# Kernel tuning notes

Hardware: AMD Instinct MI355X
Metric: run time of the kernel (lower is better)

The kernel has to match this reference:

```python
import jax, jax.numpy as jnp
import numpy as np

N_OBJ, N_REG = 4096, 8192
D_HO = D_HR = 512
GATE_W = 128
E = 131072


def setup_inputs() -> dict:
    key = jax.random.key(0)
    ks = jax.random.split(key, 10)
    s = 1.0 / np.sqrt(D_HO + D_HR)
    return {
        "feature_obj": jax.random.normal(ks[0], (N_OBJ, D_HO), jnp.float32),
        "feature_region": jax.random.normal(ks[1], (N_REG, D_HR), jnp.float32),
        # edge lists (tgt, src) equivalent to np.where(select_mat > 0)
        "r2o_tgt": jnp.sort(jax.random.randint(ks[2], (E,), 0, N_OBJ, jnp.int32)),
        "r2o_src": jax.random.randint(ks[3], (E,), 0, N_REG, jnp.int32),
        "o2r_tgt": jnp.sort(jax.random.randint(ks[4], (E,), 0, N_REG, jnp.int32)),
        "o2r_src": jax.random.randint(ks[5], (E,), 0, N_OBJ, jnp.int32),
        # attention gate Linear(dim_src+dim_tgt -> gate_width), bias=True
        "gw_r2o": jax.random.uniform(ks[6], (GATE_W, D_HR + D_HO), jnp.float32, -s, s),
        "gb_r2o": jnp.zeros((GATE_W,), jnp.float32),
        "gw_o2r": jax.random.uniform(ks[7], (GATE_W, D_HO + D_HR), jnp.float32, -s, s),
        "gb_o2r": jnp.zeros((GATE_W,), jnp.float32),
        # transform Sequential(ReLU, Linear(dim -> dim, bias=True))
        "tw_r2o": jax.random.uniform(ks[8], (D_HO, D_HR), jnp.float32, -s, s),
        "tb_r2o": jnp.zeros((D_HO,), jnp.float32),
        "tw_o2r": jax.random.uniform(ks[9], (D_HR, D_HO), jnp.float32, -s, s),
        "tb_o2r": jnp.zeros((D_HR,), jnp.float32),
    }


def _message(tgt_feat, src_feat, tgt_idx, src_idx, gw, gb, num_tgt):
    # gather per-edge source/target features: [E, ds], [E, dt]
    src = src_feat[src_idx]
    tgt = tgt_feat[tgt_idx]
    # Attention_Module: gate = mean(sigmoid(W @ relu(cat(src, tgt)) + b))
    g = jax.nn.relu(jnp.concatenate([src, tgt], axis=-1))
    gate = jnp.mean(jax.nn.sigmoid(g @ gw.T + gb), axis=-1, keepdims=True)  # [E, 1]
    msg = src * gate
    agg = jax.ops.segment_sum(msg, tgt_idx, num_segments=num_tgt)
    # mps_use_average=True -> per-target mean; targets with no edges stay zero
    cnt = jax.ops.segment_sum(jnp.ones((tgt_idx.shape[0], 1), msg.dtype), tgt_idx, num_segments=num_tgt)
    return agg / jnp.maximum(cnt, 1.0)


def reference(feature_obj, feature_region, r2o_tgt, r2o_src, o2r_tgt, o2r_src,
              gw_r2o, gb_r2o, gw_o2r, gb_o2r, tw_r2o, tb_r2o, tw_o2r, tb_o2r):
    m_r2o = _message(feature_obj, feature_region, r2o_tgt, r2o_src, gw_r2o, gb_r2o, N_OBJ)
    out_obj = feature_obj + jax.nn.relu(m_r2o) @ tw_r2o.T + tb_r2o
    m_o2r = _message(feature_region, feature_obj, o2r_tgt, o2r_src, gw_o2r, gb_o2r, N_REG)
    out_reg = feature_region + jax.nn.relu(m_o2r) @ tw_o2r.T + tb_o2r
    return (out_obj, out_reg)
```

## Files before the change

### kernel.cpp

```cpp
#include <hip/hip_runtime.h>

constexpr int N_OBJ = 4096, N_REG = 8192, D = 512, GW = 128, NE = 131072;

typedef __attribute__((ext_vector_type(8))) short short8;
typedef __attribute__((ext_vector_type(4))) float f32x4;
typedef __attribute__((ext_vector_type(2))) float f32x2;

__device__ inline short f2bf(float f) {
  unsigned u = __builtin_bit_cast(unsigned, f);
  unsigned r = (u + 0x7FFF + ((u >> 16) & 1)) >> 16;
  return (short)r;
}

__global__ __launch_bounds__(256) void cast_csr(
    const float* __restrict__ feat_reg, const float* __restrict__ feat_obj,
    const float* __restrict__ gw_r2o, const float* __restrict__ gw_o2r,
    const float* __restrict__ tw_r2o, const float* __restrict__ tw_o2r,
    const int* __restrict__ t_r2o, const int* __restrict__ t_o2r,
    unsigned char* __restrict__ raw_reg, short* __restrict__ relu_reg,
    unsigned char* __restrict__ raw_obj, short* __restrict__ relu_obj,
    short* __restrict__ Wreg, short* __restrict__ Wobj,
    short* __restrict__ btw_r2o, short* __restrict__ btw_o2r,
    int* __restrict__ off_r2o, int* __restrict__ off_o2r) {
  int i = blockIdx.x * 256 + threadIdx.x;
  if (i >= 1769472) {
    i -= 1769472;
    const int* tgt; int* off; int t;
    if (i <= N_OBJ) { tgt = t_r2o; off = off_r2o; t = i; }
    else {
      i -= N_OBJ + 1;
      if (i > N_REG) return;
      tgt = t_o2r; off = off_o2r; t = i;
    }
    int lo = 0, hi = NE;
    while (lo < hi) {
      int mid = (lo + hi) >> 1;
      if (tgt[mid] < t) lo = mid + 1; else hi = mid;
    }
    off[t] = lo;
    return;
  }
  if (i < 1572864) {
    const float* src; unsigned char* draw; short* drelu; int j = i;
    if (j < 1048576) { src = feat_reg; draw = raw_reg; drelu = relu_reg; }
    else { j -= 1048576; src = feat_obj; draw = raw_obj; drelu = relu_obj; }
    float4 v = ((const float4*)src)[j];
    int p = __builtin_amdgcn_cvt_pk_fp8_f32(v.x, v.y, 0, false);
    p = __builtin_amdgcn_cvt_pk_fp8_f32(v.z, v.w, p, true);
    ((unsigned*)draw)[j] = (unsigned)p;
    ((short4*)drelu)[j] = make_short4(f2bf(fmaxf(v.x, 0.f)), f2bf(fmaxf(v.y, 0.f)),
                                      f2bf(fmaxf(v.z, 0.f)), f2bf(fmaxf(v.w, 0.f)));
    return;
  }
  i -= 1572864;
  const float* src; short* dst; int di;
  if (i < 32768) {
    int row = i >> 7, c4 = i & 127;
    src = (row < 128) ? gw_r2o + (size_t)row * 1024 + c4 * 4
                      : gw_o2r + (size_t)(row - 128) * 1024 + 512 + c4 * 4;
    dst = Wreg; di = i;
  } else if (i < 65536) {
    int k = i - 32768, row = k >> 7, c4 = k & 127;
    src = (row < 128) ? gw_r2o + (size_t)row * 1024 + 512 + c4 * 4
                      : gw_o2r + (size_t)(row - 128) * 1024 + c4 * 4;
    dst = Wobj; di = k;
  } else if (i < 131072) { di = i - 65536; src = tw_r2o + (size_t)di * 4; dst = btw_r2o; }
  else                   { di = i - 131072; src = tw_o2r + (size_t)di * 4; dst = btw_o2r; }
  float4 v = *(const float4*)src;
  ((short4*)dst)[di] = make_short4(f2bf(v.x), f2bf(v.y), f2bf(v.z), f2bf(v.w));
}

struct GemmPair {
  const short* A[2]; const short* B[2];
  const float* res[2]; const float* bias[2];
  void* C[2];
  int nb0;
  int nxb;
  int ldc;
};

template<bool EPI, int BN>
__global__ __launch_bounds__(256) void gemm_pair(GemmPair gp) {
  constexpr int NF = BN / 32;
  __shared__ short As[2][128 * 32];
  __shared__ short Bs[2][BN * 32];
  int b = blockIdx.x;
  const int pi = (b >= gp.nb0) ? 1 : 0;
  if (pi) b -= gp.nb0;
  const int bx = b % gp.nxb, by = b / gp.nxb;
  const short* __restrict__ A = gp.A[pi];
  const short* __restrict__ B = gp.B[pi];
  const int ldc = gp.ldc;
  const int tid = threadIdx.x;
  const int lane = tid & 63, w = tid >> 6;
  const int m0 = by * 128, n0 = bx * BN;
  const int wm = (w >> 1) * 64, wn = (w & 1) * (BN / 2);
  const int sr = lane >> 2, sc = (lane & 3) * 8;
  const int fr = lane & 15, fk = (lane >> 4) * 8;

  f32x4 acc[4][NF];
#pragma unroll
  for (int i = 0; i < 4; ++i)
#pragma unroll
    for (int j = 0; j < NF; ++j) acc[i][j] = (f32x4){0.f, 0.f, 0.f, 0.f};

  auto stage = [&](int buf, int k0) {
#pragma unroll
    for (int h = 0; h < 2; ++h) {
      int rg = w * 32 + h * 16;
      const short* ga = A + (size_t)(m0 + rg + sr) * 512 + k0 + sc;
      __builtin_amdgcn_global_load_lds(
          (const __attribute__((address_space(1))) void*)ga,
          (__attribute__((address_space(3))) void*)&As[buf][rg * 32], 16, 0, 0);
    }
#pragma unroll
    for (int h = 0; h < BN / 64; ++h) {
      int rg = w * (BN / 4) + h * 16;
      const short* gb = B + (size_t)(n0 + rg + sr) * 512 + k0 + sc;
      __builtin_amdgcn_global_load_lds(
          (const __attribute__((address_space(1))) void*)gb,
          (__attribute__((address_space(3))) void*)&Bs[buf][rg * 32], 16, 0, 0);
    }
  };
  auto compute = [&](int buf) {
    short8 a[4], bb[NF];
#pragma unroll
    for (int i = 0; i < 4; ++i)
      a[i] = *(const short8*)&As[buf][(wm + i * 16 + fr) * 32 + fk];
#pragma unroll
    for (int j = 0; j < NF; ++j)
      bb[j] = *(const short8*)&Bs[buf][(wn + j * 16 + fr) * 32 + fk];
#pragma unroll
    for (int i = 0; i < 4; ++i)
#pragma unroll
      for (int j = 0; j < NF; ++j)
        acc[i][j] = __builtin_amdgcn_mfma_f32_16x16x32_bf16(a[i], bb[j], acc[i][j], 0, 0, 0);
  };

  stage(0, 0);
  __syncthreads();
  int cur = 0;
  for (int k0 = 0; k0 < 512 - 32; k0 += 32) {
    stage(cur ^ 1, k0 + 32);
    compute(cur);
    __syncthreads();
    cur ^= 1;
  }
  compute(cur);

  if (EPI) {
    float* C = (float*)gp.C[pi];
    const float* res = gp.res[pi];
    const float* bias = gp.bias[pi];
#pragma unroll
    for (int i = 0; i < 4; ++i)
#pragma unroll
      for (int j = 0; j < NF; ++j) {
        int n = n0 + wn + j * 16 + fr;
#pragma unroll
        for (int r = 0; r < 4; ++r) {
          int m = m0 + wm + i * 16 + (lane >> 4) * 4 + r;
          C[(size_t)m * ldc + n] = acc[i][j][r] + res[(size_t)m * ldc + n] + bias[n];
        }
      }
  } else {
    unsigned char* C = (unsigned char*)gp.C[pi];
#pragma unroll
    for (int i = 0; i < 4; ++i)
#pragma unroll
      for (int j = 0; j < NF; ++j) {
        int n = n0 + wn + j * 16 + fr;
#pragma unroll
        for (int r = 0; r < 4; ++r) {
          int m = m0 + wm + i * 16 + (lane >> 4) * 4 + r;
          int pk = __builtin_amdgcn_cvt_pk_fp8_f32(acc[i][j][r], acc[i][j][r], 0, false);
          C[(size_t)m * ldc + n] = (unsigned char)(pk & 0xFF);
        }
      }
  }
}

__global__ __launch_bounds__(256) void fused_msg(
    const unsigned char* __restrict__ Preg, const unsigned char* __restrict__ Pobj,
    const unsigned char* __restrict__ raw_reg, const unsigned char* __restrict__ raw_obj,
    const int* __restrict__ r2o_src, const int* __restrict__ o2r_src,
    const int* __restrict__ off_r2o, const int* __restrict__ off_o2r,
    const float* __restrict__ gb_r2o, const float* __restrict__ gb_o2r,
    short* __restrict__ m_obj, short* __restrict__ m_reg) {
  const int tid = threadIdx.x, w = tid >> 6, lane = tid & 63;
  const int q = lane >> 4, l = lane & 15;
  int t = blockIdx.x * 4 + w;
  const unsigned char *PA, *PB, *feat; const int *src, *off; const float* gb;
  short* mo; int po;
  if (t < N_OBJ) {
    PA = Preg; PB = Pobj; feat = raw_reg; src = r2o_src; off = off_r2o;
    gb = gb_r2o; mo = m_obj; po = 0;
  } else {
    t -= N_OBJ;
    PA = Pobj; PB = Preg; feat = raw_obj; src = o2r_src; off = off_o2r;
    gb = gb_o2r; mo = m_reg; po = 128;
  }
  const int e0 = off[t], e1 = off[t + 1];
  uint2 pbu = *(const uint2*)&PB[(size_t)t * 256 + po + l * 8];
  f32x2 pb0 = __builtin_amdgcn_cvt_pk_f32_fp8((int)pbu.x, false);
  f32x2 pb1 = __builtin_amdgcn_cvt_pk_f32_fp8((int)pbu.x, true);
  f32x2 pb2 = __builtin_amdgcn_cvt_pk_f32_fp8((int)pbu.y, false);
  f32x2 pb3 = __builtin_amdgcn_cvt_pk_f32_fp8((int)pbu.y, true);
  float4 gA = *(const float4*)&gb[l * 8];
  float4 gB = *(const float4*)&gb[l * 8 + 4];
  const float c0 = pb0.x + gA.x, c1 = pb0.y + gA.y;
  const float c2 = pb1.x + gA.z, c3 = pb1.y + gA.w;
  const float c4 = pb2.x + gB.x, c5 = pb2.y + gB.y;
  const float c6 = pb3.x + gB.z, c7 = pb3.y + gB.w;

  float acc[32] = {};
  for (int e = e0 + q; e < e1; e += 4) {
    int s = src[e];
    uint2 pau = *(const uint2*)&PA[(size_t)s * 256 + po + l * 8];
    uint4 f0 = *(const uint4*)&feat[(size_t)s * 512 + l * 32];
    uint4 f1 = *(const uint4*)&feat[(size_t)s * 512 + l * 32 + 16];
    f32x2 a0 = __builtin_amdgcn_cvt_pk_f32_fp8((int)pau.x, false);
    f32x2 a1 = __builtin_amdgcn_cvt_pk_f32_fp8((int)pau.x, true);
    f32x2 a2 = __builtin_amdgcn_cvt_pk_f32_fp8((int)pau.y, false);
    f32x2 a3 = __builtin_amdgcn_cvt_pk_f32_fp8((int)pau.y, true);
    float gs = __builtin_amdgcn_rcpf(1.f + __expf(-(a0.x + c0)))
             + __builtin_amdgcn_rcpf(1.f + __expf(-(a0.y + c1)))
             + __builtin_amdgcn_rcpf(1.f + __expf(-(a1.x + c2)))
             + __builtin_amdgcn_rcpf(1.f + __expf(-(a1.y + c3)))
             + __builtin_amdgcn_rcpf(1.f + __expf(-(a2.x + c4)))
             + __builtin_amdgcn_rcpf(1.f + __expf(-(a2.y + c5)))
             + __builtin_amdgcn_rcpf(1.f + __expf(-(a3.x + c6)))
             + __builtin_amdgcn_rcpf(1.f + __expf(-(a3.y + c7)));
#pragma unroll
    for (int msk = 8; msk >= 1; msk >>= 1) gs += __shfl_xor(gs, msk, 64);
    unsigned fd[8] = {f0.x, f0.y, f0.z, f0.w, f1.x, f1.y, f1.z, f1.w};
#pragma unroll
    for (int d = 0; d < 8; ++d) {
      f32x2 lo = __builtin_amdgcn_cvt_pk_f32_fp8((int)fd[d], false);
      f32x2 hi = __builtin_amdgcn_cvt_pk_f32_fp8((int)fd[d], true);
      acc[d * 4 + 0] += lo.x * gs;
      acc[d * 4 + 1] += lo.y * gs;
      acc[d * 4 + 2] += hi.x * gs;
      acc[d * 4 + 3] += hi.y * gs;
    }
  }
#pragma unroll
  for (int j = 0; j < 32; ++j) {
    acc[j] += __shfl_xor(acc[j], 16, 64);
    acc[j] += __shfl_xor(acc[j], 32, 64);
  }
  const float inv = (1.0f / 128.0f) / fmaxf((float)(e1 - e0), 1.0f);
  short8 o;
#pragma unroll
  for (int k = 0; k < 8; ++k) o[k] = f2bf(fmaxf(acc[q * 8 + k] * inv, 0.f));
  *(short8*)(mo + (size_t)t * 512 + l * 32 + q * 8) = o;
}

extern "C" void kernel_launch(void* const* d_in, const int* in_sizes, int n_in,
                              void* d_out, int out_size, void* d_ws, size_t ws_size,
                              hipStream_t stream) {
  const float* feat_obj = (const float*)d_in[0];
  const float* feat_reg = (const float*)d_in[1];
  const int*   r2o_tgt  = (const int*)d_in[2];
  const int*   r2o_src  = (const int*)d_in[3];
  const int*   o2r_tgt  = (const int*)d_in[4];
  const int*   o2r_src  = (const int*)d_in[5];
  const float* gw_r2o   = (const float*)d_in[6];
  const float* gb_r2o   = (const float*)d_in[7];
  const float* gw_o2r   = (const float*)d_in[8];
  const float* gb_o2r   = (const float*)d_in[9];
  const float* tw_r2o   = (const float*)d_in[10];
  const float* tb_r2o   = (const float*)d_in[11];
  const float* tw_o2r   = (const float*)d_in[12];
  const float* tb_o2r   = (const float*)d_in[13];
  float* out_obj = (float*)d_out;
  float* out_reg = out_obj + (size_t)N_OBJ * D;

  size_t cur = 0;
  auto alloc = [&](size_t bytes) -> void* {
    cur = (cur + 255) & ~(size_t)255;
    void* p = (char*)d_ws + cur;
    cur += bytes;
    return p;
  };
  int*   off_r2o = (int*)alloc((N_OBJ + 1) * sizeof(int));
  int*   off_o2r = (int*)alloc((N_REG + 1) * sizeof(int));
  unsigned char* raw_reg = (unsigned char*)alloc((size_t)N_REG * D);
  unsigned char* raw_obj = (unsigned char*)alloc((size_t)N_OBJ * D);
  short* relu_reg= (short*)alloc((size_t)N_REG * D * 2);
  short* relu_obj= (short*)alloc((size_t)N_OBJ * D * 2);
  short* Wreg    = (short*)alloc((size_t)256 * D * 2);
  short* Wobj    = (short*)alloc((size_t)256 * D * 2);
  short* btw_r2o = (short*)alloc((size_t)D * D * 2);
  short* btw_o2r = (short*)alloc((size_t)D * D * 2);
  unsigned char* Preg = (unsigned char*)alloc((size_t)N_REG * 256);
  unsigned char* Pobj = (unsigned char*)alloc((size_t)N_OBJ * 256);
  short* m_obj   = (short*)alloc((size_t)N_OBJ * D * 2);
  short* m_reg   = (short*)alloc((size_t)N_REG * D * 2);

  cast_csr<<<6961, 256, 0, stream>>>(feat_reg, feat_obj, gw_r2o, gw_o2r, tw_r2o, tw_o2r,
                                     r2o_tgt, o2r_tgt,
                                     raw_reg, relu_reg, raw_obj, relu_obj,
                                     Wreg, Wobj, btw_r2o, btw_o2r, off_r2o, off_o2r);

  GemmPair proj;
  proj.A[0] = relu_reg; proj.B[0] = Wreg; proj.C[0] = Preg;
  proj.A[1] = relu_obj; proj.B[1] = Wobj; proj.C[1] = Pobj;
  proj.res[0] = proj.res[1] = nullptr; proj.bias[0] = proj.bias[1] = nullptr;
  proj.nb0 = 4 * (N_REG / 128); proj.nxb = 4; proj.ldc = 256;
  gemm_pair<false, 64><<<384, 256, 0, stream>>>(proj);

  fused_msg<<<(N_OBJ + N_REG) / 4, 256, 0, stream>>>(Preg, Pobj, raw_reg, raw_obj,
                                                     r2o_src, o2r_src, off_r2o, off_o2r,
                                                     gb_r2o, gb_o2r, m_obj, m_reg);

  GemmPair tr;
  tr.A[0] = m_reg; tr.B[0] = btw_o2r; tr.res[0] = feat_reg; tr.bias[0] = tb_o2r; tr.C[0] = out_reg;
  tr.A[1] = m_obj; tr.B[1] = btw_r2o; tr.res[1] = feat_obj; tr.bias[1] = tb_r2o; tr.C[1] = out_obj;
  tr.nb0 = 4 * (N_REG / 128); tr.nxb = 4; tr.ldc = D;
  gemm_pair<true, 128><<<384, 256, 0, stream>>>(tr);
}
```

Baseline: 193.3 us.

## Split fused message kernel into per-edge gate pass and column-split aggregation

Replaces the fused per-target message kernel with two stages. A gate kernel computes one sigmoid-mean gate per edge into a float buffer, and an aggregation kernel runs twice, once per 256-column half, with each wave handling one target row and each lane covering four columns across all edges. The aim is to remove the per-edge gate recomputation inside the wide-gather loop and to use better-coalesced 4-byte feature loads per lane. The cost is an extra gate buffer round trip through memory, two more kernel launches, and src indices being read three times.

```diff
diff --git a/kernel.cpp b/kernel.cpp
--- a/kernel.cpp
+++ b/kernel.cpp
@@ -74,9 +74,7 @@
   const short* A[2]; const short* B[2];
   const float* res[2]; const float* bias[2];
   void* C[2];
-  int nb0;
-  int nxb;
-  int ldc;
+  int nb0, nxb, ldc;
 };
 
 template<bool EPI, int BN>
@@ -180,80 +178,88 @@
   }
 }
 
-__global__ __launch_bounds__(256) void fused_msg(
+__global__ __launch_bounds__(256) void gate_k(
     const unsigned char* __restrict__ Preg, const unsigned char* __restrict__ Pobj,
+    const int* __restrict__ r2o_tgt, const int* __restrict__ r2o_src,
+    const int* __restrict__ o2r_tgt, const int* __restrict__ o2r_src,
+    const float* __restrict__ gb_r2o, const float* __restrict__ gb_o2r,
+    float* __restrict__ gate_r2o, float* __restrict__ gate_o2r) {
+  const int tid = threadIdx.x, l = tid & 31;
+  const int e = blockIdx.x * 8 + (tid >> 5);
+  const unsigned char *pa, *pb; const float* gb; float* out;
+  if (blockIdx.y == 0) {
+    pa = Preg + (size_t)r2o_src[e] * 256 + l * 4;
+    pb = Pobj + (size_t)r2o_tgt[e] * 256 + l * 4;
+    gb = gb_r2o; out = gate_r2o;
+  } else {
+    pa = Pobj + (size_t)o2r_src[e] * 256 + 128 + l * 4;
+    pb = Preg + (size_t)o2r_tgt[e] * 256 + 128 + l * 4;
+    gb = gb_o2r; out = gate_o2r;
+  }
+  unsigned pau = *(const unsigned*)pa;
+  unsigned pbu = *(const unsigned*)pb;
+  float4 gbv = *(const float4*)&gb[l * 4];
+  f32x2 a01 = __builtin_amdgcn_cvt_pk_f32_fp8((int)pau, false);
+  f32x2 a23 = __builtin_amdgcn_cvt_pk_f32_fp8((int)pau, true);
+  f32x2 b01 = __builtin_amdgcn_cvt_pk_f32_fp8((int)pbu, false);
+  f32x2 b23 = __builtin_amdgcn_cvt_pk_f32_fp8((int)pbu, true);
+  float gs = __builtin_amdgcn_rcpf(1.f + __expf(-(a01.x + b01.x + gbv.x)))
+           + __builtin_amdgcn_rcpf(1.f + __expf(-(a01.y + b01.y + gbv.y)))
+           + __builtin_amdgcn_rcpf(1.f + __expf(-(a23.x + b23.x + gbv.z)))
+           + __builtin_amdgcn_rcpf(1.f + __expf(-(a23.y + b23.y + gbv.w)));
+#pragma unroll
+  for (int msk = 16; msk >= 1; msk >>= 1) gs += __shfl_xor(gs, msk, 64);
+  if (l == 0) out[e] = gs * (1.0f / 128.0f);
+}
+
+__global__ __launch_bounds__(256) void acc_k(
     const unsigned char* __restrict__ raw_reg, const unsigned char* __restrict__ raw_obj,
+    const float* __restrict__ gate_r2o, const float* __restrict__ gate_o2r,
     const int* __restrict__ r2o_src, const int* __restrict__ o2r_src,
     const int* __restrict__ off_r2o, const int* __restrict__ off_o2r,
-    const float* __restrict__ gb_r2o, const float* __restrict__ gb_o2r,
-    short* __restrict__ m_obj, short* __restrict__ m_reg) {
+    short* __restrict__ m_obj, short* __restrict__ m_reg, int off) {
   const int tid = threadIdx.x, w = tid >> 6, lane = tid & 63;
-  const int q = lane >> 4, l = lane & 15;
   int t = blockIdx.x * 4 + w;
-  const unsigned char *PA, *PB, *feat; const int *src, *off; const float* gb;
-  short* mo; int po;
+  const unsigned char* feat; const float* gate; const int *src, *offs; short* mo;
   if (t < N_OBJ) {
-    PA = Preg; PB = Pobj; feat = raw_reg; src = r2o_src; off = off_r2o;
-    gb = gb_r2o; mo = m_obj; po = 0;
+    feat = raw_reg; gate = gate_r2o; src = r2o_src; offs = off_r2o; mo = m_obj;
   } else {
     t -= N_OBJ;
-    PA = Pobj; PB = Preg; feat = raw_obj; src = o2r_src; off = off_o2r;
-    gb = gb_o2r; mo = m_reg; po = 128;
-  }
-  const int e0 = off[t], e1 = off[t + 1];
-  uint2 pbu = *(const uint2*)&PB[(size_t)t * 256 + po + l * 8];
-  f32x2 pb0 = __builtin_amdgcn_cvt_pk_f32_fp8((int)pbu.x, false);
-  f32x2 pb1 = __builtin_amdgcn_cvt_pk_f32_fp8((int)pbu.x, true);
-  f32x2 pb2 = __builtin_amdgcn_cvt_pk_f32_fp8((int)pbu.y, false);
-  f32x2 pb3 = __builtin_amdgcn_cvt_pk_f32_fp8((int)pbu.y, true);
-  float4 gA = *(const float4*)&gb[l * 8];
-  float4 gB = *(const float4*)&gb[l * 8 + 4];
-  const float c0 = pb0.x + gA.x, c1 = pb0.y + gA.y;
-  const float c2 = pb1.x + gA.z, c3 = pb1.y + gA.w;
-  const float c4 = pb2.x + gB.x, c5 = pb2.y + gB.y;
-  const float c6 = pb3.x + gB.z, c7 = pb3.y + gB.w;
-
-  float acc[32] = {};
-  for (int e = e0 + q; e < e1; e += 4) {
+    feat = raw_obj; gate = gate_o2r; src = o2r_src; offs = off_o2r; mo = m_reg;
+  }
+  const int e0 = offs[t], e1 = offs[t + 1];
+  const unsigned char* fbase = feat + off + lane * 4;
+  float a0 = 0.f, a1 = 0.f, a2 = 0.f, a3 = 0.f;
+  int e = e0;
+  for (; e + 1 < e1; e += 2) {
+    int s0 = src[e], s1 = src[e + 1];
+    float g0 = gate[e], g1 = gate[e + 1];
+    unsigned u0 = *(const unsigned*)(fbase + (size_t)s0 * 512);
+    unsigned u1 = *(const unsigned*)(fbase + (size_t)s1 * 512);
+    f32x2 lo0 = __builtin_amdgcn_cvt_pk_f32_fp8((int)u0, false);
+    f32x2 hi0 = __builtin_amdgcn_cvt_pk_f32_fp8((int)u0, true);
+    f32x2 lo1 = __builtin_amdgcn_cvt_pk_f32_fp8((int)u1, false);
+    f32x2 hi1 = __builtin_amdgcn_cvt_pk_f32_fp8((int)u1, true);
+    a0 += lo0.x * g0 + lo1.x * g1;
+    a1 += lo0.y * g0 + lo1.y * g1;
+    a2 += hi0.x * g0 + hi1.x * g1;
+    a3 += hi0.y * g0 + hi1.y * g1;
+  }
+  if (e < e1) {
     int s = src[e];
-    uint2 pau = *(const uint2*)&PA[(size_t)s * 256 + po + l * 8];
-    uint4 f0 = *(const uint4*)&feat[(size_t)s * 512 + l * 32];
-    uint4 f1 = *(const uint4*)&feat[(size_t)s * 512 + l * 32 + 16];
-    f32x2 a0 = __builtin_amdgcn_cvt_pk_f32_fp8((int)pau.x, false);
-    f32x2 a1 = __builtin_amdgcn_cvt_pk_f32_fp8((int)pau.x, true);
-    f32x2 a2 = __builtin_amdgcn_cvt_pk_f32_fp8((int)pau.y, false);
-    f32x2 a3 = __builtin_amdgcn_cvt_pk_f32_fp8((int)pau.y, true);
-    float gs = __builtin_amdgcn_rcpf(1.f + __expf(-(a0.x + c0)))
-             + __builtin_amdgcn_rcpf(1.f + __expf(-(a0.y + c1)))
-             + __builtin_amdgcn_rcpf(1.f + __expf(-(a1.x + c2)))
-             + __builtin_amdgcn_rcpf(1.f + __expf(-(a1.y + c3)))
-             + __builtin_amdgcn_rcpf(1.f + __expf(-(a2.x + c4)))
-             + __builtin_amdgcn_rcpf(1.f + __expf(-(a2.y + c5)))
-             + __builtin_amdgcn_rcpf(1.f + __expf(-(a3.x + c6)))
-             + __builtin_amdgcn_rcpf(1.f + __expf(-(a3.y + c7)));
-#pragma unroll
-    for (int msk = 8; msk >= 1; msk >>= 1) gs += __shfl_xor(gs, msk, 64);
-    unsigned fd[8] = {f0.x, f0.y, f0.z, f0.w, f1.x, f1.y, f1.z, f1.w};
-#pragma unroll
-    for (int d = 0; d < 8; ++d) {
-      f32x2 lo = __builtin_amdgcn_cvt_pk_f32_fp8((int)fd[d], false);
-      f32x2 hi = __builtin_amdgcn_cvt_pk_f32_fp8((int)fd[d], true);
-      acc[d * 4 + 0] += lo.x * gs;
-      acc[d * 4 + 1] += lo.y * gs;
-      acc[d * 4 + 2] += hi.x * gs;
-      acc[d * 4 + 3] += hi.y * gs;
-    }
-  }
-#pragma unroll
-  for (int j = 0; j < 32; ++j) {
-    acc[j] += __shfl_xor(acc[j], 16, 64);
-    acc[j] += __shfl_xor(acc[j], 32, 64);
-  }
-  const float inv = (1.0f / 128.0f) / fmaxf((float)(e1 - e0), 1.0f);
-  short8 o;
-#pragma unroll
-  for (int k = 0; k < 8; ++k) o[k] = f2bf(fmaxf(acc[q * 8 + k] * inv, 0.f));
-  *(short8*)(mo + (size_t)t * 512 + l * 32 + q * 8) = o;
+    float g = gate[e];
+    unsigned u = *(const unsigned*)(fbase + (size_t)s * 512);
+    f32x2 lo = __builtin_amdgcn_cvt_pk_f32_fp8((int)u, false);
+    f32x2 hi = __builtin_amdgcn_cvt_pk_f32_fp8((int)u, true);
+    a0 += lo.x * g; a1 += lo.y * g; a2 += hi.x * g; a3 += hi.y * g;
+  }
+  const float inv = 1.0f / fmaxf((float)(e1 - e0), 1.0f);
+  short4 o;
+  o.x = f2bf(fmaxf(a0 * inv, 0.f));
+  o.y = f2bf(fmaxf(a1 * inv, 0.f));
+  o.z = f2bf(fmaxf(a2 * inv, 0.f));
+  o.w = f2bf(fmaxf(a3 * inv, 0.f));
+  *(short4*)(mo + (size_t)t * 512 + off + lane * 4) = o;
 }
 
 extern "C" void kernel_launch(void* const* d_in, const int* in_sizes, int n_in,
@@ -295,6 +301,8 @@
   short* btw_o2r = (short*)alloc((size_t)D * D * 2);
   unsigned char* Preg = (unsigned char*)alloc((size_t)N_REG * 256);
   unsigned char* Pobj = (unsigned char*)alloc((size_t)N_OBJ * 256);
+  float* gate_r2o= (float*)alloc((size_t)NE * 4);
+  float* gate_o2r= (float*)alloc((size_t)NE * 4);
   short* m_obj   = (short*)alloc((size_t)N_OBJ * D * 2);
   short* m_reg   = (short*)alloc((size_t)N_REG * D * 2);
 
@@ -310,9 +318,15 @@
   proj.nb0 = 4 * (N_REG / 128); proj.nxb = 4; proj.ldc = 256;
   gemm_pair<false, 64><<<384, 256, 0, stream>>>(proj);
 
-  fused_msg<<<(N_OBJ + N_REG) / 4, 256, 0, stream>>>(Preg, Pobj, raw_reg, raw_obj,
-                                                     r2o_src, o2r_src, off_r2o, off_o2r,
-                                                     gb_r2o, gb_o2r, m_obj, m_reg);
+  gate_k<<<dim3(NE / 8, 2), 256, 0, stream>>>(Preg, Pobj, r2o_tgt, r2o_src, o2r_tgt, o2r_src,
+                                              gb_r2o, gb_o2r, gate_r2o, gate_o2r);
+
+  acc_k<<<(N_OBJ + N_REG) / 4, 256, 0, stream>>>(raw_reg, raw_obj, gate_r2o, gate_o2r,
+                                                 r2o_src, o2r_src, off_r2o, off_o2r,
+                                                 m_obj, m_reg, 0);
+  acc_k<<<(N_OBJ + N_REG) / 4, 256, 0, stream>>>(raw_reg, raw_obj, gate_r2o, gate_o2r,
+                                                 r2o_src, o2r_src, off_r2o, off_o2r,
+                                                 m_obj, m_reg, 256);
 
   GemmPair tr;
   tr.A[0] = m_reg; tr.B[0] = btw_o2r; tr.res[0] = feat_reg; tr.bias[0] = tb_o2r; tr.C[0] = out_reg;
```

After: 212.8 us. 1.1x slower.
